# Optimization experiments

Hardware: AMD Instinct MI355X
Metric: run time of the kernel (lower is better)

Reference implementation:

```python
import jax, jax.numpy as jnp
import numpy as np

B, S, D, H = 2, 2048, 1024, 16
DK = D // H


def setup_inputs() -> dict:
    key = jax.random.key(0)
    ks = jax.random.split(key, 11)
    scale = jnp.float32(1.0 / np.sqrt(D))
    inp = {
        "query": jax.random.normal(ks[0], (B, S, D), jnp.float32),
        "key": jax.random.normal(ks[1], (B, S, D), jnp.float32),
        "value": jax.random.normal(ks[2], (B, S, D), jnp.float32),
        # causal mask: True = masked (masked_fill semantics), broadcast over batch/heads
        "mask": jnp.triu(jnp.ones((S, S), dtype=bool), k=1)[None, None, :, :],
        "Wq": jax.random.normal(ks[3], (D, D), jnp.float32) * scale,
        "bq": jnp.zeros((D,), jnp.float32),
        "Wk": jax.random.normal(ks[4], (D, D), jnp.float32) * scale,
        "bk": jnp.zeros((D,), jnp.float32),
        "Wv": jax.random.normal(ks[5], (D, D), jnp.float32) * scale,
        "bv": jnp.zeros((D,), jnp.float32),
        "Wo": jax.random.normal(ks[6], (D, D), jnp.float32) * scale,
        "bo": jnp.zeros((D,), jnp.float32),
    }
    return inp


def _split_heads(x):
    # (B, S, D) -> (B, H, S, DK)
    b, s, _ = x.shape
    return x.reshape(b, s, H, DK).transpose(0, 2, 1, 3)


def reference(query, key, value, mask, Wq, bq, Wk, bk, Wv, bv, Wo, bo):
    # nn.Linear: y = x @ W.T + b
    q = _split_heads(query @ Wq.T + bq)
    k = _split_heads(key @ Wk.T + bk)
    v = _split_heads(value @ Wv.T + bv)

    inv_sqrt_dk = jnp.float32(1.0 / np.sqrt(DK))
    scores = jnp.einsum("bhqd,bhkd->bhqk", q, k) * inv_sqrt_dk  # (B,H,S,S)
    scores = jnp.where(mask, jnp.float32(-jnp.inf), scores)
    weights = jax.nn.softmax(scores, axis=-1)
    weights = jnp.nan_to_num(weights, nan=0.0)  # fully-masked rows -> 0

    attn = jnp.einsum("bhqk,bhkd->bhqd", weights, v)  # (B,H,S,DK)
    merged = attn.transpose(0, 2, 1, 3).reshape(B, S, D)  # merge heads
    return merged @ Wo.T + bo
```

## Files before the change

### kernel.cpp

```cpp
#include <hip/hip_runtime.h>


typedef unsigned short u16;
typedef unsigned int u32;
typedef __attribute__((ext_vector_type(8))) __bf16 bf16x8;
typedef __attribute__((ext_vector_type(8))) unsigned short us8;
typedef __attribute__((ext_vector_type(4))) float f32x4;

#define S_LEN 2048
#define D_DIM 1024
#define NH 16
#define DKH 64
#define Mi 1048576ULL

__device__ __forceinline__ u16 f2bf(float f) {
  return __builtin_bit_cast(u16, (__bf16)f);
}
__device__ __forceinline__ bf16x8 ld_frag(const u16* p) {
  us8 v = *(const us8*)p;
  return __builtin_bit_cast(bf16x8, v);
}
__device__ __forceinline__ void gl2lds16(const u16* g, u16* l) {
  __builtin_amdgcn_global_load_lds(
      (__attribute__((address_space(1))) void*)(g),
      (__attribute__((address_space(3))) void*)(l), 16, 0, 0);
}

__global__ __launch_bounds__(256, 1) void cvt_all(
    const float* __restrict__ q, const float* __restrict__ k, const float* __restrict__ v,
    const float* __restrict__ wq, const float* __restrict__ wk,
    const float* __restrict__ wv, const float* __restrict__ wo,
    u16* __restrict__ dst)
{
  size_t e0 = ((size_t)blockIdx.x * 256 + threadIdx.x) * 8;
  const float* s;
  if      (e0 <  4*Mi) s = q  + e0;
  else if (e0 <  8*Mi) s = k  + (e0 - 4*Mi);
  else if (e0 < 12*Mi) s = v  + (e0 - 8*Mi);
  else if (e0 < 13*Mi) s = wq + (e0 - 12*Mi);
  else if (e0 < 14*Mi) s = wk + (e0 - 13*Mi);
  else if (e0 < 15*Mi) s = wv + (e0 - 14*Mi);
  else                 s = wo + (e0 - 15*Mi);
  float4 a = ((const float4*)s)[0];
  float4 b = ((const float4*)s)[1];
  us8 o;
  o[0]=f2bf(a.x); o[1]=f2bf(a.y); o[2]=f2bf(a.z); o[3]=f2bf(a.w);
  o[4]=f2bf(b.x); o[5]=f2bf(b.y); o[6]=f2bf(b.z); o[7]=f2bf(b.w);
  *(us8*)(dst + e0) = o;
}

__global__ __launch_bounds__(256, 1) void gemm_qkv_bb(
    const u16* __restrict__ Aq, const u16* __restrict__ Ak, const u16* __restrict__ Av,
    const u16* __restrict__ Wqb, const u16* __restrict__ Wkb, const u16* __restrict__ Wvb,
    const float* __restrict__ bq, const float* __restrict__ bk, const float* __restrict__ bv,
    u16* __restrict__ Oq, u16* __restrict__ Ok, u16* __restrict__ Ov, float qscale)
{
  const int z = blockIdx.z;
  const u16* A = (z == 0) ? Aq : (z == 1) ? Ak : Av;
  const u16* W = (z == 0) ? Wqb : (z == 1) ? Wkb : Wvb;
  const float* bias = (z == 0) ? bq : (z == 1) ? bk : bv;
  u16* out = (z == 0) ? Oq : (z == 1) ? Ok : Ov;
  const float scale = (z == 0) ? qscale : 1.0f;
  const int K = 1024;

  __shared__ u16 lA[128 * 32];
  __shared__ u16 lB[128 * 32];
  const int t = threadIdx.x;
  const int w = t >> 6, l = t & 63;
  const int mblk = blockIdx.y * 128, nblk = blockIdx.x * 128;
  const int wm = (w & 1) * 64, wn = (w >> 1) * 64;
  const int lr = l & 15, lq = l >> 4;
  const int srow = l >> 2, scol = (l & 3) * 8;

  f32x4 acc[4][4] = {};

  for (int k0 = 0; k0 < K; k0 += 32) {
    __syncthreads();
    #pragma unroll
    for (int r = 0; r < 2; ++r) {
      int grp = r * 4 + w;
      gl2lds16(A + (size_t)(mblk + grp * 16 + srow) * K + k0 + scol, &lA[grp * 512]);
      gl2lds16(W + (size_t)(nblk + grp * 16 + srow) * K + k0 + scol, &lB[grp * 512]);
    }
    __syncthreads();
    bf16x8 aF[4], bF[4];
    #pragma unroll
    for (int mt = 0; mt < 4; ++mt)
      aF[mt] = ld_frag(&lA[(wm + mt * 16 + lr) * 32 + lq * 8]);
    #pragma unroll
    for (int nt = 0; nt < 4; ++nt)
      bF[nt] = ld_frag(&lB[(wn + nt * 16 + lr) * 32 + lq * 8]);
    #pragma unroll
    for (int mt = 0; mt < 4; ++mt)
      #pragma unroll
      for (int nt = 0; nt < 4; ++nt)
        acc[mt][nt] = __builtin_amdgcn_mfma_f32_16x16x32_bf16(aF[mt], bF[nt], acc[mt][nt], 0, 0, 0);
  }

  #pragma unroll
  for (int mt = 0; mt < 4; ++mt)
    #pragma unroll
    for (int nt = 0; nt < 4; ++nt)
      #pragma unroll
      for (int r = 0; r < 4; ++r) {
        int rowg = mblk + wm + mt * 16 + lq * 4 + r;
        int colg = nblk + wn + nt * 16 + lr;
        float v = (acc[mt][nt][r] + bias[colg]) * scale;
        int b = rowg >> 11, s = rowg & 2047;
        int h = colg >> 6, dk = colg & 63;
        if (z != 2)
          out[(((size_t)(b * NH + h)) * S_LEN + s) * DKH + dk] = f2bf(v);
        else
          out[(((size_t)(b * NH + h)) * DKH + dk) * S_LEN + s] = f2bf(v);
      }
}

__global__ __launch_bounds__(256, 1) void gemm_out_bb(
    const u16* __restrict__ A, const u16* __restrict__ W,
    const float* __restrict__ bias, float* __restrict__ out)
{
  const int K = 1024;
  __shared__ u16 lA[128 * 32];
  __shared__ u16 lB[64 * 32];
  const int t = threadIdx.x;
  const int w = t >> 6, l = t & 63;
  const int mblk = blockIdx.y * 128, nblk = blockIdx.x * 64;
  const int wm = (w & 1) * 64, wn = (w >> 1) * 32;
  const int lr = l & 15, lq = l >> 4;
  const int srow = l >> 2, scol = (l & 3) * 8;

  f32x4 acc[4][2] = {};

  for (int k0 = 0; k0 < K; k0 += 32) {
    __syncthreads();
    #pragma unroll
    for (int r = 0; r < 2; ++r) {
      int grp = r * 4 + w;
      gl2lds16(A + (size_t)(mblk + grp * 16 + srow) * K + k0 + scol, &lA[grp * 512]);
    }
    gl2lds16(W + (size_t)(nblk + w * 16 + srow) * K + k0 + scol, &lB[w * 512]);
    __syncthreads();
    bf16x8 aF[4], bF[2];
    #pragma unroll
    for (int mt = 0; mt < 4; ++mt)
      aF[mt] = ld_frag(&lA[(wm + mt * 16 + lr) * 32 + lq * 8]);
    #pragma unroll
    for (int nt = 0; nt < 2; ++nt)
      bF[nt] = ld_frag(&lB[(wn + nt * 16 + lr) * 32 + lq * 8]);
    #pragma unroll
    for (int mt = 0; mt < 4; ++mt)
      #pragma unroll
      for (int nt = 0; nt < 2; ++nt)
        acc[mt][nt] = __builtin_amdgcn_mfma_f32_16x16x32_bf16(aF[mt], bF[nt], acc[mt][nt], 0, 0, 0);
  }

  #pragma unroll
  for (int mt = 0; mt < 4; ++mt)
    #pragma unroll
    for (int nt = 0; nt < 2; ++nt)
      #pragma unroll
      for (int r = 0; r < 4; ++r) {
        int rowg = mblk + wm + mt * 16 + lq * 4 + r;
        int colg = nblk + wn + nt * 16 + lr;
        out[(size_t)rowg * D_DIM + colg] = acc[mt][nt][r] + bias[colg];
      }
}

__global__ __launch_bounds__(256, 1) void attn_fused(
    const u16* __restrict__ Q, const u16* __restrict__ K,
    const u16* __restrict__ Vt, u16* __restrict__ O)
{
  __shared__ u16 lK[2][64 * 64];
  __shared__ u16 lV[2][64 * 64];

  const int idx = blockIdx.x;
  const int s_ = idx >> 8;
  const int r_ = idx & 255;
  const int bh = r_ & 31;
  const int t_ = r_ >> 5;
  const int qt = (s_ == 0) ? t_ : (s_ == 1) ? 31 - t_ : (s_ == 2) ? 8 + t_ : 23 - t_;
  const int b = bh >> 4, h = bh & 15;
  const int t = threadIdx.x;
  const int w = t >> 6, l = t & 63;
  const int lr = l & 15, lq = l >> 4;

  const u16* Qp = Q + (size_t)bh * S_LEN * DKH;
  const u16* Kp = K + (size_t)bh * S_LEN * DKH;
  const u16* Vp = Vt + (size_t)bh * DKH * S_LEN;

  const int srow8 = l >> 3;
  const int schunk = l & 7;

  const int qrow = qt * 64 + w * 16 + lr;
  bf16x8 qf[2];
  qf[0] = ld_frag(Qp + (size_t)qrow * DKH + lq * 8);
  qf[1] = ld_frag(Qp + (size_t)qrow * DKH + 32 + lq * 8);

  f32x4 o[4] = {};
  f32x4 li4 = {};

  #pragma unroll
  for (int r2 = 0; r2 < 2; ++r2) {
    int grp = r2 * 4 + w;
    int row = grp * 8 + srow8;
    int sw = (row & 3) | (((row >> 3) & 1) << 2);
    int c = schunk ^ sw;
    gl2lds16(Kp + (size_t)row * DKH + c * 8, &lK[0][grp * 512]);
    gl2lds16(Vp + (size_t)row * S_LEN + c * 8, &lV[0][grp * 512]);
  }

  for (int kt = 0; kt <= qt; ++kt) {
    const int cur = kt & 1;
    __syncthreads();

    if (kt < qt) {
      #pragma unroll
      for (int r2 = 0; r2 < 2; ++r2) {
        int grp = r2 * 4 + w;
        int row = grp * 8 + srow8;
        int sw = (row & 3) | (((row >> 3) & 1) << 2);
        int c = schunk ^ sw;
        gl2lds16(Kp + (size_t)((kt + 1) * 64 + row) * DKH + c * 8, &lK[cur ^ 1][grp * 512]);
        gl2lds16(Vp + (size_t)row * S_LEN + (kt + 1) * 64 + c * 8, &lV[cur ^ 1][grp * 512]);
      }
    }

    f32x4 st[4] = {};
    #pragma unroll
    for (int ksd = 0; ksd < 2; ++ksd)
      #pragma unroll
      for (int nt = 0; nt < 4; ++nt) {
        int sig = 32 * (nt >> 1) + 8 * (lr >> 2) + 4 * (nt & 1) + (lr & 3);
        int slot = (ksd * 4 + lq) ^ (lr & 7);
        bf16x8 kb = ld_frag(&lK[cur][sig * 64 + slot * 8]);
        st[nt] = __builtin_amdgcn_mfma_f32_16x16x32_bf16(kb, qf[ksd], st[nt], 0, 0, 0);
      }

    float p[4][4];
    const bool diag = (kt == qt);
    const int qloc = w * 16 + lr;
    #pragma unroll
    for (int nt = 0; nt < 4; ++nt)
      #pragma unroll
      for (int r = 0; r < 4; ++r) {
        int kk = 32 * (nt >> 1) + 8 * lq + 4 * (nt & 1) + r;
        float e = exp2f(st[nt][r]);
        p[nt][r] = (diag && kk > qloc) ? 0.0f : e;
        li4[r] += p[nt][r];
      }

    #pragma unroll
    for (int ks = 0; ks < 2; ++ks) {
      us8 av;
      #pragma unroll
      for (int j = 0; j < 4; ++j) {
        av[j] = f2bf(p[2 * ks][j]);
        av[4 + j] = f2bf(p[2 * ks + 1][j]);
      }
      bf16x8 pa = __builtin_bit_cast(bf16x8, av);
      #pragma unroll
      for (int dblk = 0; dblk < 4; ++dblk) {
        int d = dblk * 16 + lr;
        int sw = (d & 3) | (((d >> 3) & 1) << 2);
        int slot = (4 * ks + lq) ^ sw;
        bf16x8 vb = ld_frag(&lV[cur][d * 64 + slot * 8]);
        o[dblk] = __builtin_amdgcn_mfma_f32_16x16x32_bf16(pa, vb, o[dblk], 0, 0, 0);
      }
    }
  }

  float li = li4[0] + li4[1] + li4[2] + li4[3];
  li += __shfl_xor(li, 16);
  li += __shfl_xor(li, 32);
  float ri[4];
  #pragma unroll
  for (int r = 0; r < 4; ++r) ri[r] = 1.0f / __shfl(li, lq * 4 + r);

  const size_t obase = ((size_t)b * S_LEN + qt * 64 + w * 16) * D_DIM + h * DKH;
  #pragma unroll
  for (int dblk = 0; dblk < 4; ++dblk)
    #pragma unroll
    for (int r = 0; r < 4; ++r)
      O[obase + (size_t)(lq * 4 + r) * D_DIM + dblk * 16 + lr] = f2bf(o[dblk][r] * ri[r]);
}

extern "C" void kernel_launch(void* const* d_in, const int* in_sizes, int n_in,
                              void* d_out, int out_size, void* d_ws, size_t ws_size,
                              hipStream_t stream) {
  const float* query = (const float*)d_in[0];
  const float* key   = (const float*)d_in[1];
  const float* value = (const float*)d_in[2];
  const float* Wq = (const float*)d_in[4];
  const float* bq = (const float*)d_in[5];
  const float* Wk = (const float*)d_in[6];
  const float* bk = (const float*)d_in[7];
  const float* Wv = (const float*)d_in[8];
  const float* bv = (const float*)d_in[9];
  const float* Wo = (const float*)d_in[10];
  const float* bo = (const float*)d_in[11];
  float* out = (float*)d_out;

  const float qscale = 0.125f * 1.44269504088896341f;
  dim3 blk(256);

  u16* base = (u16*)d_ws;
  u16* Qb = base;
  u16* Kb = base + 4 * Mi;
  u16* Vb = base + 8 * Mi;

  u16* cvt = base + 12 * Mi;
  u16* qbf = cvt;
  u16* kbf = cvt + 4 * Mi;
  u16* vbf = cvt + 8 * Mi;
  u16* wqb = cvt + 12 * Mi;
  u16* wkb = cvt + 13 * Mi;
  u16* wvb = cvt + 14 * Mi;
  u16* wob = cvt + 15 * Mi;
  u16* Ab  = qbf;

  cvt_all<<<dim3(8192), blk, 0, stream>>>(query, key, value, Wq, Wk, Wv, Wo, cvt);
  gemm_qkv_bb<<<dim3(8, 32, 3), blk, 0, stream>>>(qbf, kbf, vbf, wqb, wkb, wvb,
                                                  bq, bk, bv, Qb, Kb, Vb, qscale);
  attn_fused<<<dim3(1024), blk, 0, stream>>>(Qb, Kb, Vb, Ab);
  gemm_out_bb<<<dim3(16, 32), blk, 0, stream>>>(Ab, wob, bo, out);
}
```

Before: 233.5 us.

## Double-buffer LDS tiles in projection GEMMs and enlarge output GEMM tile

Both bf16 GEMM kernels now use two LDS stages. The next K-slice is prefetched with global_load_lds while the current slice feeds the MFMAs, which cuts the two barriers per iteration down to one and lets global loads overlap compute. Block indices are remapped so consecutive blocks walk along M while sharing the same N column of weights, aiming for better L2 reuse. The output projection moves from 128x64 to 128x128 tiles, launching half as many blocks. This doubles LDS use and relies on the barrier's implicit wait for the async LDS loads to finish.

New measurement: 241.6 us. +3.5%, slower.

```diff
diff --git a/kernel.cpp b/kernel.cpp
--- a/kernel.cpp
+++ b/kernel.cpp
@@ -63,33 +63,43 @@
   const float scale = (z == 0) ? qscale : 1.0f;
   const int K = 1024;
 
-  __shared__ u16 lA[128 * 32];
-  __shared__ u16 lB[128 * 32];
+  __shared__ u16 lA[2][128 * 32];
+  __shared__ u16 lB[2][128 * 32];
   const int t = threadIdx.x;
   const int w = t >> 6, l = t & 63;
-  const int mblk = blockIdx.y * 128, nblk = blockIdx.x * 128;
+  const int lin = blockIdx.x + 8 * blockIdx.y;
+  const int mblk = (lin & 31) * 128, nblk = (lin >> 5) * 128;
   const int wm = (w & 1) * 64, wn = (w >> 1) * 64;
   const int lr = l & 15, lq = l >> 4;
   const int srow = l >> 2, scol = (l & 3) * 8;
 
   f32x4 acc[4][4] = {};
 
-  for (int k0 = 0; k0 < K; k0 += 32) {
+  #pragma unroll
+  for (int r = 0; r < 2; ++r) {
+    int grp = r * 4 + w;
+    gl2lds16(A + (size_t)(mblk + grp * 16 + srow) * K + scol, &lA[0][grp * 512]);
+    gl2lds16(W + (size_t)(nblk + grp * 16 + srow) * K + scol, &lB[0][grp * 512]);
+  }
+
+  for (int k0 = 0, it = 0; k0 < K; k0 += 32, ++it) {
+    const int cur = it & 1;
     __syncthreads();
-    #pragma unroll
-    for (int r = 0; r < 2; ++r) {
-      int grp = r * 4 + w;
-      gl2lds16(A + (size_t)(mblk + grp * 16 + srow) * K + k0 + scol, &lA[grp * 512]);
-      gl2lds16(W + (size_t)(nblk + grp * 16 + srow) * K + k0 + scol, &lB[grp * 512]);
+    if (k0 + 32 < K) {
+      #pragma unroll
+      for (int r = 0; r < 2; ++r) {
+        int grp = r * 4 + w;
+        gl2lds16(A + (size_t)(mblk + grp * 16 + srow) * K + k0 + 32 + scol, &lA[cur ^ 1][grp * 512]);
+        gl2lds16(W + (size_t)(nblk + grp * 16 + srow) * K + k0 + 32 + scol, &lB[cur ^ 1][grp * 512]);
+      }
     }
-    __syncthreads();
     bf16x8 aF[4], bF[4];
     #pragma unroll
     for (int mt = 0; mt < 4; ++mt)
-      aF[mt] = ld_frag(&lA[(wm + mt * 16 + lr) * 32 + lq * 8]);
-    #pragma unroll
-    for (int nt = 0; nt < 4; ++nt)
-      bF[nt] = ld_frag(&lB[(wn + nt * 16 + lr) * 32 + lq * 8]);
+      aF[mt] = ld_frag(&lA[cur][(wm + mt * 16 + lr) * 32 + lq * 8]);
+    #pragma unroll
+    for (int nt = 0; nt < 4; ++nt)
+      bF[nt] = ld_frag(&lB[cur][(wn + nt * 16 + lr) * 32 + lq * 8]);
     #pragma unroll
     for (int mt = 0; mt < 4; ++mt)
       #pragma unroll
@@ -120,44 +130,54 @@
     const float* __restrict__ bias, float* __restrict__ out)
 {
   const int K = 1024;
-  __shared__ u16 lA[128 * 32];
-  __shared__ u16 lB[64 * 32];
+  __shared__ u16 lA[2][128 * 32];
+  __shared__ u16 lB[2][128 * 32];
   const int t = threadIdx.x;
   const int w = t >> 6, l = t & 63;
-  const int mblk = blockIdx.y * 128, nblk = blockIdx.x * 64;
-  const int wm = (w & 1) * 64, wn = (w >> 1) * 32;
+  const int lin = blockIdx.x + 8 * blockIdx.y;
+  const int mblk = (lin & 31) * 128, nblk = (lin >> 5) * 128;
+  const int wm = (w & 1) * 64, wn = (w >> 1) * 64;
   const int lr = l & 15, lq = l >> 4;
   const int srow = l >> 2, scol = (l & 3) * 8;
 
-  f32x4 acc[4][2] = {};
-
-  for (int k0 = 0; k0 < K; k0 += 32) {
+  f32x4 acc[4][4] = {};
+
+  #pragma unroll
+  for (int r = 0; r < 2; ++r) {
+    int grp = r * 4 + w;
+    gl2lds16(A + (size_t)(mblk + grp * 16 + srow) * K + scol, &lA[0][grp * 512]);
+    gl2lds16(W + (size_t)(nblk + grp * 16 + srow) * K + scol, &lB[0][grp * 512]);
+  }
+
+  for (int k0 = 0, it = 0; k0 < K; k0 += 32, ++it) {
+    const int cur = it & 1;
     __syncthreads();
-    #pragma unroll
-    for (int r = 0; r < 2; ++r) {
-      int grp = r * 4 + w;
-      gl2lds16(A + (size_t)(mblk + grp * 16 + srow) * K + k0 + scol, &lA[grp * 512]);
+    if (k0 + 32 < K) {
+      #pragma unroll
+      for (int r = 0; r < 2; ++r) {
+        int grp = r * 4 + w;
+        gl2lds16(A + (size_t)(mblk + grp * 16 + srow) * K + k0 + 32 + scol, &lA[cur ^ 1][grp * 512]);
+        gl2lds16(W + (size_t)(nblk + grp * 16 + srow) * K + k0 + 32 + scol, &lB[cur ^ 1][grp * 512]);
+      }
     }
-    gl2lds16(W + (size_t)(nblk + w * 16 + srow) * K + k0 + scol, &lB[w * 512]);
-    __syncthreads();
-    bf16x8 aF[4], bF[2];
+    bf16x8 aF[4], bF[4];
     #pragma unroll
     for (int mt = 0; mt < 4; ++mt)
-      aF[mt] = ld_frag(&lA[(wm + mt * 16 + lr) * 32 + lq * 8]);
-    #pragma unroll
-    for (int nt = 0; nt < 2; ++nt)
-      bF[nt] = ld_frag(&lB[(wn + nt * 16 + lr) * 32 + lq * 8]);
+      aF[mt] = ld_frag(&lA[cur][(wm + mt * 16 + lr) * 32 + lq * 8]);
+    #pragma unroll
+    for (int nt = 0; nt < 4; ++nt)
+      bF[nt] = ld_frag(&lB[cur][(wn + nt * 16 + lr) * 32 + lq * 8]);
     #pragma unroll
     for (int mt = 0; mt < 4; ++mt)
       #pragma unroll
-      for (int nt = 0; nt < 2; ++nt)
+      for (int nt = 0; nt < 4; ++nt)
         acc[mt][nt] = __builtin_amdgcn_mfma_f32_16x16x32_bf16(aF[mt], bF[nt], acc[mt][nt], 0, 0, 0);
   }
 
   #pragma unroll
   for (int mt = 0; mt < 4; ++mt)
     #pragma unroll
-    for (int nt = 0; nt < 2; ++nt)
+    for (int nt = 0; nt < 4; ++nt)
       #pragma unroll
       for (int r = 0; r < 4; ++r) {
         int rowg = mblk + wm + mt * 16 + lq * 4 + r;
@@ -322,5 +342,5 @@
   gemm_qkv_bb<<<dim3(8, 32, 3), blk, 0, stream>>>(qbf, kbf, vbf, wqb, wkb, wvb,
                                                   bq, bk, bv, Qb, Kb, Vb, qscale);
   attn_fused<<<dim3(1024), blk, 0, stream>>>(Qb, Kb, Vb, Ab);
-  gemm_out_bb<<<dim3(16, 32), blk, 0, stream>>>(Ab, wob, bo, out);
-}
+  gemm_out_bb<<<dim3(8, 32), blk, 0, stream>>>(Ab, wob, bo, out);
+}
```
